# Performance work log

Hardware: AMD Instinct MI355X
Metric: run time of the kernel (lower is better)

Reference implementation:

```python
import jax, jax.numpy as jnp
import numpy as np

D_MODEL = 256
NHEAD = 8
HEAD_DIM = D_MODEL // NHEAD
CLIP = 10.0


def setup_inputs() -> dict:
    key = jax.random.key(0)
    k1, k2, k3, k4 = jax.random.split(key, 4)
    B, N = 4, 256
    nodes = jax.random.normal(k1, (B, N, D_MODEL), dtype=jnp.float32)
    edges = jax.random.normal(k2, (B, N, N, D_MODEL), dtype=jnp.float32)
    # torch nn.Linear default init: U(-1/sqrt(in), 1/sqrt(in))
    bound = 1.0 / np.sqrt(D_MODEL)
    W = jax.random.uniform(k3, (D_MODEL, D_MODEL), minval=-bound, maxval=bound, dtype=jnp.float32)
    b = jax.random.uniform(k4, (D_MODEL,), minval=-bound, maxval=bound, dtype=jnp.float32)
    return {"nodes": nodes, "edges": edges, "W": W, "b": b}


def reference(nodes, edges, W, b):
    B, N, _ = nodes.shape
    H, Dh = NHEAD, HEAD_DIM

    def proj(x):  # torch Linear: x @ W.T + b
        return x @ W.T + b

    # Node projections: the module applies the SAME linear to q, k, v
    node_p = proj(nodes).reshape(B, N, H, Dh)
    nq, nk, nv = node_p, node_p, node_p
    # Edge projections (same linear for q and k)
    edge_p = proj(edges).reshape(B, N, N, H, Dh)
    eq, ek = edge_p, edge_p

    query = eq + nq[:, :, None, :, :]   # (B,N,N,H,Dh)
    key = ek + nk[:, None, :, :, :]     # (B,N,N,H,Dh)
    scores = jnp.einsum('bijhd,bijhd->bhij', query, key) / np.sqrt(Dh).astype(np.float32)
    scores = CLIP * jnp.tanh(scores)
    attn = jax.nn.softmax(scores, axis=-1)  # (B,H,N,N)
    # output = attn @ values (values transposed to (B,H,N,Dh))
    out = jnp.einsum('bhij,bjhd->bihd', attn, nv).reshape(B, N, D_MODEL)
    out = proj(out)
    return (out, attn)
```

## Files before the change

### kernel.cpp

```cpp
#include <hip/hip_runtime.h>
#include <math.h>

typedef short short8 __attribute__((ext_vector_type(8)));
typedef float f32x4 __attribute__((ext_vector_type(4)));

__device__ __forceinline__ unsigned short f2bf(float x) {
    unsigned u = __float_as_uint(x);
    u += 0x7FFF + ((u >> 16) & 1);
    return (unsigned short)(u >> 16);
}
__device__ __forceinline__ float bf2f(unsigned short h) {
    return __uint_as_float(((unsigned)h) << 16);
}

__global__ __launch_bounds__(256) void k_prep(const float* __restrict__ W,
                                              float* __restrict__ Wt,
                                              unsigned short* __restrict__ Whi,
                                              unsigned short* __restrict__ Wlo) {
    int d = blockIdx.x, k = threadIdx.x;
    float w = W[d * 256 + k];
    Wt[k * 256 + d] = w;
    unsigned short hi = f2bf(w);
    Whi[d * 256 + k] = hi;
    Wlo[d * 256 + k] = f2bf(w - bf2f(hi));
}

__global__ __launch_bounds__(256) void k_node_proj(const float* __restrict__ nodes,
                                                   const float* __restrict__ Wt,
                                                   const float* __restrict__ bias,
                                                   float* __restrict__ np_) {
    int row = blockIdx.x;
    int d = threadIdx.x;
    __shared__ float xl[256];
    xl[d] = nodes[row * 256 + d];
    __syncthreads();
    float a0 = 0.f, a1 = 0.f, a2 = 0.f, a3 = 0.f;
#pragma unroll 8
    for (int k = 0; k < 256; k += 4) {
        a0 = fmaf(xl[k],     Wt[(k)     * 256 + d], a0);
        a1 = fmaf(xl[k + 1], Wt[(k + 1) * 256 + d], a1);
        a2 = fmaf(xl[k + 2], Wt[(k + 2) * 256 + d], a2);
        a3 = fmaf(xl[k + 3], Wt[(k + 3) * 256 + d], a3);
    }
    np_[row * 256 + d] = bias[d] + (a0 + a1) + (a2 + a3);
}

#define LDSW 40

__global__ __launch_bounds__(256) void k_edge_mfma(const float* __restrict__ edges,
                                                   const unsigned short* __restrict__ Whi,
                                                   const unsigned short* __restrict__ Wlo,
                                                   const float* __restrict__ bias,
                                                   const float* __restrict__ np_,
                                                   float* __restrict__ attn) {
    __shared__ unsigned short Eh[64 * LDSW], El[64 * LDSW];
    __shared__ unsigned short Wh[256 * LDSW], Wl[256 * LDSW];
    __shared__ float npi[256];
    __shared__ float sc[8][64];

    const int t = threadIdx.x;
    const int w = t >> 6, l = t & 63;
    const int m0 = blockIdx.x * 64;
    const int bb = m0 >> 16, ii = (m0 >> 8) & 255, j0 = m0 & 255;

    if (t < 64) ((float4*)npi)[t] = ((const float4*)(np_ + (size_t)(bb * 256 + ii) * 256))[t];

    f32x4 acc[4][4];
#pragma unroll
    for (int mt = 0; mt < 4; ++mt)
#pragma unroll
        for (int nt = 0; nt < 4; ++nt) acc[mt][nt] = (f32x4){0.f, 0.f, 0.f, 0.f};

    const int er = t >> 2, eo = t & 3;
    const float* egbase = edges + (size_t)(m0 + er) * 256 + eo * 8;
    const int col = l & 15, g = l >> 4;

    for (int kc = 0; kc < 8; ++kc) {
        __syncthreads();
        {
            float4 v0 = *(const float4*)(egbase + kc * 32);
            float4 v1 = *(const float4*)(egbase + kc * 32 + 4);
            float f[8] = {v0.x, v0.y, v0.z, v0.w, v1.x, v1.y, v1.z, v1.w};
            short8 hi, lo;
#pragma unroll
            for (int q = 0; q < 8; ++q) {
                unsigned short h = f2bf(f[q]);
                hi[q] = (short)h;
                lo[q] = (short)f2bf(f[q] - bf2f(h));
            }
            *(short8*)(Eh + er * LDSW + eo * 8) = hi;
            *(short8*)(El + er * LDSW + eo * 8) = lo;
        }
#pragma unroll
        for (int s = 0; s < 4; ++s) {
            int idx = t + s * 256;
            int d = idx >> 2, o = idx & 3;
            *(short8*)(Wh + d * LDSW + o * 8) =
                *(const short8*)(Whi + d * 256 + kc * 32 + o * 8);
            *(short8*)(Wl + d * LDSW + o * 8) =
                *(const short8*)(Wlo + d * 256 + kc * 32 + o * 8);
        }
        __syncthreads();
        short8 Ah[4], Al[4];
#pragma unroll
        for (int mt = 0; mt < 4; ++mt) {
            Ah[mt] = *(const short8*)(Eh + (mt * 16 + col) * LDSW + g * 8);
            Al[mt] = *(const short8*)(El + (mt * 16 + col) * LDSW + g * 8);
        }
#pragma unroll
        for (int nt = 0; nt < 4; ++nt) {
            int nrow = w * 64 + nt * 16 + col;
            short8 Bh = *(const short8*)(Wh + nrow * LDSW + g * 8);
            short8 Bl = *(const short8*)(Wl + nrow * LDSW + g * 8);
#pragma unroll
            for (int mt = 0; mt < 4; ++mt) {
                acc[mt][nt] = __builtin_amdgcn_mfma_f32_16x16x32_bf16(Ah[mt], Bh, acc[mt][nt], 0, 0, 0);
                acc[mt][nt] = __builtin_amdgcn_mfma_f32_16x16x32_bf16(Ah[mt], Bl, acc[mt][nt], 0, 0, 0);
                acc[mt][nt] = __builtin_amdgcn_mfma_f32_16x16x32_bf16(Al[mt], Bh, acc[mt][nt], 0, 0, 0);
            }
        }
    }

    const float isq = 0.17677669529663687f;
    float bv[4], nv[4];
#pragma unroll
    for (int nt = 0; nt < 4; ++nt) {
        int d = w * 64 + nt * 16 + col;
        bv[nt] = bias[d];
        nv[nt] = npi[d];
    }
#pragma unroll
    for (int mt = 0; mt < 4; ++mt) {
#pragma unroll
        for (int r = 0; r < 4; ++r) {
            int el = mt * 16 + g * 4 + r;
            int j = j0 + el;
            const float* npj = np_ + (size_t)(bb * 256 + j) * 256 + w * 64;
            float p0 = acc[mt][0][r] + bv[0];
            float p1 = acc[mt][1][r] + bv[1];
            float p2 = acc[mt][2][r] + bv[2];
            float p3 = acc[mt][3][r] + bv[3];
            float s0 = (p0 + nv[0]) * (p0 + npj[col]) +
                       (p1 + nv[1]) * (p1 + npj[16 + col]);
            float s1 = (p2 + nv[2]) * (p2 + npj[32 + col]) +
                       (p3 + nv[3]) * (p3 + npj[48 + col]);
#pragma unroll
            for (int m = 1; m < 16; m <<= 1) {
                s0 += __shfl_xor(s0, m, 64);
                s1 += __shfl_xor(s1, m, 64);
            }
            if (col == 0) {
                sc[2 * w][el]     = 10.f * tanhf(s0 * isq);
                sc[2 * w + 1][el] = 10.f * tanhf(s1 * isq);
            }
        }
    }
    __syncthreads();
    if (t < 128) {
        int h = t >> 4, q = t & 15;
        float4 v = *(float4*)&sc[h][q * 4];
        *(float4*)(attn + (((size_t)(bb * 8 + h) * 256 + ii) << 8) + j0 + q * 4) = v;
    }
}

__global__ __launch_bounds__(256) void k_softmax(float* __restrict__ attn) {
    int row = (blockIdx.x * 256 + threadIdx.x) >> 6;
    int lane = threadIdx.x & 63;
    float4* rowp = (float4*)(attn + (size_t)row * 256);
    float4 v = rowp[lane];
    float m = fmaxf(fmaxf(v.x, v.y), fmaxf(v.z, v.w));
#pragma unroll
    for (int s = 1; s < 64; s <<= 1) m = fmaxf(m, __shfl_xor(m, s, 64));
    v.x = expf(v.x - m); v.y = expf(v.y - m);
    v.z = expf(v.z - m); v.w = expf(v.w - m);
    float sum = v.x + v.y + v.z + v.w;
#pragma unroll
    for (int s = 1; s < 64; s <<= 1) sum += __shfl_xor(sum, s, 64);
    float inv = 1.f / sum;
    v.x *= inv; v.y *= inv; v.z *= inv; v.w *= inv;
    rowp[lane] = v;
}

__global__ __launch_bounds__(256) void k_out(const float* __restrict__ attn,
                                             const float* __restrict__ np_,
                                             const float* __restrict__ Wt,
                                             const float* __restrict__ bias,
                                             float* __restrict__ out) {
    int bi = blockIdx.x;
    int bb = bi >> 8, ii = bi & 255;
    int d = threadIdx.x;
    __shared__ float at[8 * 256];
    __shared__ float xl[256];
#pragma unroll
    for (int s = 0; s < 2; ++s) {
        int idx = d + s * 256;
        int h = idx >> 6, q = idx & 63;
        ((float4*)at)[idx] =
            ((const float4*)(attn + ((size_t)(bb * 8 + h) * 256 + ii) * 256))[q];
    }
    __syncthreads();
    int h = d >> 5;
    const float* npb = np_ + (size_t)bb * 65536 + d;
    const float* ath = at + h * 256;
    float a0 = 0.f, a1 = 0.f, a2 = 0.f, a3 = 0.f;
#pragma unroll 4
    for (int j = 0; j < 256; j += 4) {
        a0 = fmaf(ath[j],     npb[(size_t)(j)     * 256], a0);
        a1 = fmaf(ath[j + 1], npb[(size_t)(j + 1) * 256], a1);
        a2 = fmaf(ath[j + 2], npb[(size_t)(j + 2) * 256], a2);
        a3 = fmaf(ath[j + 3], npb[(size_t)(j + 3) * 256], a3);
    }
    xl[d] = (a0 + a1) + (a2 + a3);
    __syncthreads();
    float c0 = bias[d], c1 = 0.f, c2 = 0.f, c3 = 0.f;
#pragma unroll 4
    for (int k = 0; k < 256; k += 4) {
        c0 = fmaf(xl[k],     Wt[(k)     * 256 + d], c0);
        c1 = fmaf(xl[k + 1], Wt[(k + 1) * 256 + d], c1);
        c2 = fmaf(xl[k + 2], Wt[(k + 2) * 256 + d], c2);
        c3 = fmaf(xl[k + 3], Wt[(k + 3) * 256 + d], c3);
    }
    out[bi * 256 + d] = (c0 + c1) + (c2 + c3);
}

extern "C" void kernel_launch(void* const* d_in, const int* in_sizes, int n_in,
                              void* d_out, int out_size, void* d_ws, size_t ws_size,
                              hipStream_t stream) {
    (void)in_sizes; (void)n_in; (void)out_size; (void)ws_size;
    const float* nodes = (const float*)d_in[0];
    const float* edges = (const float*)d_in[1];
    const float* W     = (const float*)d_in[2];
    const float* bias  = (const float*)d_in[3];

    float* out  = (float*)d_out;
    float* attn = out + 262144;

    float* np_ = (float*)d_ws;
    float* Wt  = np_ + 262144;
    unsigned short* Whi = (unsigned short*)(Wt + 65536);
    unsigned short* Wlo = Whi + 65536;

    hipLaunchKernelGGL(k_prep,      dim3(256),  dim3(256), 0, stream, W, Wt, Whi, Wlo);
    hipLaunchKernelGGL(k_node_proj, dim3(1024), dim3(256), 0, stream, nodes, Wt, bias, np_);
    hipLaunchKernelGGL(k_edge_mfma, dim3(4096), dim3(256), 0, stream, edges, Whi, Wlo, bias, np_, attn);
    hipLaunchKernelGGL(k_softmax,   dim3(2048), dim3(256), 0, stream, attn);
    hipLaunchKernelGGL(k_out,       dim3(1024), dim3(256), 0, stream, attn, np_, Wt, bias, out);
}
```

Before: 547.4 us.

## Retile edge MFMA kernel to 128x128 tiles with prefetch and async W loads

Each edge-projection block now computes a 128-row by 128-column tile, so two blocks split the output columns and each reads its 128 edge rows. The next K-chunk of edges is prefetched into registers, and W hi/lo slices go straight into LDS via global_load_lds. The change also uses packed bf16 conversion, an exp-based tanh and __expf in softmax, and wider accumulator unrolling in the node-projection and output kernels. In exchange, every edge row is fetched by two blocks, and the unpadded LDS layout may cause bank conflicts.

```diff
diff --git a/kernel.cpp b/kernel.cpp
--- a/kernel.cpp
+++ b/kernel.cpp
@@ -1,4 +1,5 @@
 #include <hip/hip_runtime.h>
+#include <hip/hip_bf16.h>
 #include <math.h>
 
 typedef short short8 __attribute__((ext_vector_type(8)));
@@ -12,6 +13,31 @@
 __device__ __forceinline__ float bf2f(unsigned short h) {
     return __uint_as_float(((unsigned)h) << 16);
 }
+
+__device__ __forceinline__ void cvt2(float f0, float f1,
+                                     unsigned short& h0, unsigned short& h1,
+                                     unsigned short& l0, unsigned short& l1) {
+    __hip_bfloat162 h = __float22bfloat162_rn(float2{f0, f1});
+    unsigned hu = *(unsigned*)&h;
+    h0 = (unsigned short)(hu & 0xFFFFu);
+    h1 = (unsigned short)(hu >> 16);
+    float r0 = f0 - __uint_as_float((hu & 0xFFFFu) << 16);
+    float r1 = f1 - __uint_as_float(hu & 0xFFFF0000u);
+    __hip_bfloat162 lo = __float22bfloat162_rn(float2{r0, r1});
+    unsigned lu = *(unsigned*)&lo;
+    l0 = (unsigned short)(lu & 0xFFFFu);
+    l1 = (unsigned short)(lu >> 16);
+}
+
+__device__ __forceinline__ float tanh10(float y) {
+    float e = __expf(2.f * y);
+    return 10.f * (e - 1.f) / (e + 1.f);
+}
+
+#define GLDS16(gp, lp)                                                        \
+    __builtin_amdgcn_global_load_lds(                                         \
+        (const __attribute__((address_space(1))) void*)(gp),                  \
+        (__attribute__((address_space(3))) void*)(lp), 16, 0, 0)
 
 __global__ __launch_bounds__(256) void k_prep(const float* __restrict__ W,
                                               float* __restrict__ Wt,
@@ -34,18 +60,16 @@
     __shared__ float xl[256];
     xl[d] = nodes[row * 256 + d];
     __syncthreads();
-    float a0 = 0.f, a1 = 0.f, a2 = 0.f, a3 = 0.f;
-#pragma unroll 8
-    for (int k = 0; k < 256; k += 4) {
-        a0 = fmaf(xl[k],     Wt[(k)     * 256 + d], a0);
-        a1 = fmaf(xl[k + 1], Wt[(k + 1) * 256 + d], a1);
-        a2 = fmaf(xl[k + 2], Wt[(k + 2) * 256 + d], a2);
-        a3 = fmaf(xl[k + 3], Wt[(k + 3) * 256 + d], a3);
-    }
-    np_[row * 256 + d] = bias[d] + (a0 + a1) + (a2 + a3);
-}
-
-#define LDSW 40
+    float a[8] = {0.f, 0.f, 0.f, 0.f, 0.f, 0.f, 0.f, 0.f};
+#pragma unroll 4
+    for (int k = 0; k < 256; k += 8) {
+#pragma unroll
+        for (int q = 0; q < 8; ++q)
+            a[q] = fmaf(xl[k + q], Wt[(k + q) * 256 + d], a[q]);
+    }
+    np_[row * 256 + d] =
+        bias[d] + ((a[0] + a[1]) + (a[2] + a[3])) + ((a[4] + a[5]) + (a[6] + a[7]));
+}
 
 __global__ __launch_bounds__(256) void k_edge_mfma(const float* __restrict__ edges,
                                                    const unsigned short* __restrict__ Whi,
@@ -53,17 +77,23 @@
                                                    const float* __restrict__ bias,
                                                    const float* __restrict__ np_,
                                                    float* __restrict__ attn) {
-    __shared__ unsigned short Eh[64 * LDSW], El[64 * LDSW];
-    __shared__ unsigned short Wh[256 * LDSW], Wl[256 * LDSW];
-    __shared__ float npi[256];
-    __shared__ float sc[8][64];
+    __shared__ unsigned short Eh[128 * 32], El[128 * 32];
+    __shared__ unsigned short Wh[128 * 32], Wl[128 * 32];
+    __shared__ float npi[128];
+    __shared__ float sc[4][128];
 
     const int t = threadIdx.x;
     const int w = t >> 6, l = t & 63;
-    const int m0 = blockIdx.x * 64;
-    const int bb = m0 >> 16, ii = (m0 >> 8) & 255, j0 = m0 & 255;
-
-    if (t < 64) ((float4*)npi)[t] = ((const float4*)(np_ + (size_t)(bb * 256 + ii) * 256))[t];
+    const int tile = blockIdx.x >> 1;
+    const int half = blockIdx.x & 1;
+    const int m0 = tile * 128;
+    const int bb = m0 >> 16;
+    const int ii = (m0 >> 8) & 255;
+    const int j0 = m0 & 255;
+    const int n0 = half * 128;
+
+    if (t < 32)
+        ((float4*)npi)[t] = ((const float4*)(np_ + (size_t)(bb * 256 + ii) * 256 + n0))[t];
 
     f32x4 acc[4][4];
 #pragma unroll
@@ -71,47 +101,59 @@
 #pragma unroll
         for (int nt = 0; nt < 4; ++nt) acc[mt][nt] = (f32x4){0.f, 0.f, 0.f, 0.f};
 
-    const int er = t >> 2, eo = t & 3;
-    const float* egbase = edges + (size_t)(m0 + er) * 256 + eo * 8;
+    const int er = t >> 1, ehk = t & 1;
+    const float* esrc = edges + (size_t)(m0 + er) * 256 + ehk * 16;
+
+    const int wrow = (l >> 2), wq = l & 3;
+
     const int col = l & 15, g = l >> 4;
+    const int wm = (w & 1) * 64, wn = (w >> 1) * 64;
+
+    float4 ecur[4], enext[4];
+#pragma unroll
+    for (int q = 0; q < 4; ++q) ecur[q] = *(const float4*)(esrc + q * 4);
 
     for (int kc = 0; kc < 8; ++kc) {
-        __syncthreads();
+#pragma unroll
+        for (int s = 0; s < 2; ++s) {
+            int base = w * 32 + s * 16;
+            const unsigned short* gh =
+                Whi + (size_t)(n0 + base + wrow) * 256 + kc * 32 + wq * 8;
+            const unsigned short* gl =
+                Wlo + (size_t)(n0 + base + wrow) * 256 + kc * 32 + wq * 8;
+            GLDS16(gh, Wh + base * 32);
+            GLDS16(gl, Wl + base * 32);
+        }
         {
-            float4 v0 = *(const float4*)(egbase + kc * 32);
-            float4 v1 = *(const float4*)(egbase + kc * 32 + 4);
-            float f[8] = {v0.x, v0.y, v0.z, v0.w, v1.x, v1.y, v1.z, v1.w};
-            short8 hi, lo;
-#pragma unroll
-            for (int q = 0; q < 8; ++q) {
-                unsigned short h = f2bf(f[q]);
-                hi[q] = (short)h;
-                lo[q] = (short)f2bf(f[q] - bf2f(h));
-            }
-            *(short8*)(Eh + er * LDSW + eo * 8) = hi;
-            *(short8*)(El + er * LDSW + eo * 8) = lo;
-        }
-#pragma unroll
-        for (int s = 0; s < 4; ++s) {
-            int idx = t + s * 256;
-            int d = idx >> 2, o = idx & 3;
-            *(short8*)(Wh + d * LDSW + o * 8) =
-                *(const short8*)(Whi + d * 256 + kc * 32 + o * 8);
-            *(short8*)(Wl + d * LDSW + o * 8) =
-                *(const short8*)(Wlo + d * 256 + kc * 32 + o * 8);
+            unsigned short hi[16], lo[16];
+#pragma unroll
+            for (int q = 0; q < 4; ++q) {
+                cvt2(ecur[q].x, ecur[q].y, hi[q * 4 + 0], hi[q * 4 + 1],
+                     lo[q * 4 + 0], lo[q * 4 + 1]);
+                cvt2(ecur[q].z, ecur[q].w, hi[q * 4 + 2], hi[q * 4 + 3],
+                     lo[q * 4 + 2], lo[q * 4 + 3]);
+            }
+            *(short8*)(Eh + er * 32 + ehk * 16)     = *(short8*)&hi[0];
+            *(short8*)(Eh + er * 32 + ehk * 16 + 8) = *(short8*)&hi[8];
+            *(short8*)(El + er * 32 + ehk * 16)     = *(short8*)&lo[0];
+            *(short8*)(El + er * 32 + ehk * 16 + 8) = *(short8*)&lo[8];
+        }
+        if (kc < 7) {
+#pragma unroll
+            for (int q = 0; q < 4; ++q)
+                enext[q] = *(const float4*)(esrc + (kc + 1) * 32 + q * 4);
         }
         __syncthreads();
         short8 Ah[4], Al[4];
 #pragma unroll
         for (int mt = 0; mt < 4; ++mt) {
-            Ah[mt] = *(const short8*)(Eh + (mt * 16 + col) * LDSW + g * 8);
-            Al[mt] = *(const short8*)(El + (mt * 16 + col) * LDSW + g * 8);
+            Ah[mt] = *(const short8*)(Eh + (wm + mt * 16 + col) * 32 + g * 8);
+            Al[mt] = *(const short8*)(El + (wm + mt * 16 + col) * 32 + g * 8);
         }
 #pragma unroll
         for (int nt = 0; nt < 4; ++nt) {
-            int nrow = w * 64 + nt * 16 + col;
-            short8 Bh = *(const short8*)(Wh + nrow * LDSW + g * 8);
-            short8 Bl = *(const short8*)(Wl + nrow * LDSW + g * 8);
+            short8 Bh = *(const short8*)(Wh + (wn + nt * 16 + col) * 32 + g * 8);
+            short8 Bl = *(const short8*)(Wl + (wn + nt * 16 + col) * 32 + g * 8);
 #pragma unroll
             for (int mt = 0; mt < 4; ++mt) {
                 acc[mt][nt] = __builtin_amdgcn_mfma_f32_16x16x32_bf16(Ah[mt], Bh, acc[mt][nt], 0, 0, 0);
@@ -119,23 +161,27 @@
                 acc[mt][nt] = __builtin_amdgcn_mfma_f32_16x16x32_bf16(Al[mt], Bh, acc[mt][nt], 0, 0, 0);
             }
         }
+        __syncthreads();
+#pragma unroll
+        for (int q = 0; q < 4; ++q) ecur[q] = enext[q];
     }
 
     const float isq = 0.17677669529663687f;
     float bv[4], nv[4];
 #pragma unroll
     for (int nt = 0; nt < 4; ++nt) {
-        int d = w * 64 + nt * 16 + col;
-        bv[nt] = bias[d];
-        nv[nt] = npi[d];
-    }
+        int dl = wn + nt * 16 + col;
+        bv[nt] = bias[n0 + dl];
+        nv[nt] = npi[dl];
+    }
+    const int hl0 = (w >> 1) * 2;
 #pragma unroll
     for (int mt = 0; mt < 4; ++mt) {
 #pragma unroll
         for (int r = 0; r < 4; ++r) {
-            int el = mt * 16 + g * 4 + r;
+            int el = wm + mt * 16 + g * 4 + r;
             int j = j0 + el;
-            const float* npj = np_ + (size_t)(bb * 256 + j) * 256 + w * 64;
+            const float* npj = np_ + (size_t)(bb * 256 + j) * 256 + n0 + wn;
             float p0 = acc[mt][0][r] + bv[0];
             float p1 = acc[mt][1][r] + bv[1];
             float p2 = acc[mt][2][r] + bv[2];
@@ -150,16 +196,16 @@
                 s1 += __shfl_xor(s1, m, 64);
             }
             if (col == 0) {
-                sc[2 * w][el]     = 10.f * tanhf(s0 * isq);
-                sc[2 * w + 1][el] = 10.f * tanhf(s1 * isq);
+                sc[hl0][el]     = tanh10(s0 * isq);
+                sc[hl0 + 1][el] = tanh10(s1 * isq);
             }
         }
     }
     __syncthreads();
     if (t < 128) {
-        int h = t >> 4, q = t & 15;
-        float4 v = *(float4*)&sc[h][q * 4];
-        *(float4*)(attn + (((size_t)(bb * 8 + h) * 256 + ii) << 8) + j0 + q * 4) = v;
+        int hl = t >> 5, q = t & 31;
+        float4 v = *(float4*)&sc[hl][q * 4];
+        *(float4*)(attn + (((size_t)(bb * 8 + half * 4 + hl) * 256 + ii) << 8) + j0 + q * 4) = v;
     }
 }
 
@@ -171,8 +217,8 @@
     float m = fmaxf(fmaxf(v.x, v.y), fmaxf(v.z, v.w));
 #pragma unroll
     for (int s = 1; s < 64; s <<= 1) m = fmaxf(m, __shfl_xor(m, s, 64));
-    v.x = expf(v.x - m); v.y = expf(v.y - m);
-    v.z = expf(v.z - m); v.w = expf(v.w - m);
+    v.x = __expf(v.x - m); v.y = __expf(v.y - m);
+    v.z = __expf(v.z - m); v.w = __expf(v.w - m);
     float sum = v.x + v.y + v.z + v.w;
 #pragma unroll
     for (int s = 1; s < 64; s <<= 1) sum += __shfl_xor(sum, s, 64);
@@ -202,25 +248,24 @@
     int h = d >> 5;
     const float* npb = np_ + (size_t)bb * 65536 + d;
     const float* ath = at + h * 256;
-    float a0 = 0.f, a1 = 0.f, a2 = 0.f, a3 = 0.f;
-#pragma unroll 4
-    for (int j = 0; j < 256; j += 4) {
-        a0 = fmaf(ath[j],     npb[(size_t)(j)     * 256], a0);
-        a1 = fmaf(ath[j + 1], npb[(size_t)(j + 1) * 256], a1);
-        a2 = fmaf(ath[j + 2], npb[(size_t)(j + 2) * 256], a2);
-        a3 = fmaf(ath[j + 3], npb[(size_t)(j + 3) * 256], a3);
-    }
-    xl[d] = (a0 + a1) + (a2 + a3);
-    __syncthreads();
-    float c0 = bias[d], c1 = 0.f, c2 = 0.f, c3 = 0.f;
-#pragma unroll 4
-    for (int k = 0; k < 256; k += 4) {
-        c0 = fmaf(xl[k],     Wt[(k)     * 256 + d], c0);
-        c1 = fmaf(xl[k + 1], Wt[(k + 1) * 256 + d], c1);
-        c2 = fmaf(xl[k + 2], Wt[(k + 2) * 256 + d], c2);
-        c3 = fmaf(xl[k + 3], Wt[(k + 3) * 256 + d], c3);
-    }
-    out[bi * 256 + d] = (c0 + c1) + (c2 + c3);
+    float a[8] = {0.f, 0.f, 0.f, 0.f, 0.f, 0.f, 0.f, 0.f};
+#pragma unroll 2
+    for (int j = 0; j < 256; j += 8) {
+#pragma unroll
+        for (int q = 0; q < 8; ++q)
+            a[q] = fmaf(ath[j + q], npb[(size_t)(j + q) * 256], a[q]);
+    }
+    xl[d] = ((a[0] + a[1]) + (a[2] + a[3])) + ((a[4] + a[5]) + (a[6] + a[7]));
+    __syncthreads();
+    float c[8] = {bias[d], 0.f, 0.f, 0.f, 0.f, 0.f, 0.f, 0.f};
+#pragma unroll 2
+    for (int k = 0; k < 256; k += 8) {
+#pragma unroll
+        for (int q = 0; q < 8; ++q)
+            c[q] = fmaf(xl[k + q], Wt[(k + q) * 256 + d], c[q]);
+    }
+    out[bi * 256 + d] =
+        ((c[0] + c[1]) + (c[2] + c[3])) + ((c[4] + c[5]) + (c[6] + c[7]));
 }
 
 extern "C" void kernel_launch(void* const* d_in, const int* in_sizes, int n_in,
```

New measurement: 529.6 us. 1.03x faster.
